# Kernel tuning notes

Hardware: AMD Instinct MI355X
Metric: run time of the kernel (lower is better)

Reference implementation:

```python
import jax, jax.numpy as jnp
import numpy as np

N_NODES = 100000
N_EDGES = 1600000
IN_DIM = 75
H_COMP = 64
H_BOND = 16
DEPTH = 3


def setup_inputs() -> dict:
    key = jax.random.key(0)
    ks = jax.random.split(key, 8)
    x = jax.random.normal(ks[0], (N_NODES, IN_DIM), dtype=jnp.float32)
    edge_index = jax.random.randint(ks[1], (2, N_EDGES), 0, N_NODES, dtype=jnp.int64)
    edge_attr = jax.random.normal(ks[2], (N_EDGES, H_BOND), dtype=jnp.float32)
    proj_w = jax.random.normal(ks[3], (IN_DIM, H_COMP), dtype=jnp.float32) * (1.0 / np.sqrt(IN_DIM))
    proj_b = jnp.zeros((H_COMP,), dtype=jnp.float32)
    u2_w = jax.random.normal(ks[4], (DEPTH, H_COMP + H_BOND, H_COMP), dtype=jnp.float32) * (1.0 / np.sqrt(H_COMP + H_BOND))
    u2_b = jnp.zeros((DEPTH, H_COMP), dtype=jnp.float32)
    u1_w = jax.random.normal(ks[5], (DEPTH, 2 * H_COMP, H_COMP), dtype=jnp.float32) * (1.0 / np.sqrt(2 * H_COMP))
    u1_b = jnp.zeros((DEPTH, H_COMP), dtype=jnp.float32)
    return {"x": x, "edge_index": edge_index, "edge_attr": edge_attr,
            "proj_w": proj_w, "proj_b": proj_b,
            "u2_w": u2_w, "u2_b": u2_b, "u1_w": u1_w, "u1_b": u1_b}


def reference(x, edge_index, edge_attr, proj_w, proj_b, u2_w, u2_b, u1_w, u1_b):
    # PyG default flow source_to_target: messages gathered from edge_index[0],
    # scatter-added at edge_index[1].
    src, dst = edge_index[0], edge_index[1]
    n = x.shape[0]
    # input projection: [N, in_dim] -> [N, H]
    h = x @ proj_w + proj_b
    for l in range(u2_w.shape[0]):
        # message: concat(x_j, edge_attr) -> Linear -> LeakyReLU(0.1)   [E, H+B] -> [E, H]
        z = jnp.concatenate([h[src], edge_attr], axis=-1)
        m = jax.nn.leaky_relu(z @ u2_w[l] + u2_b[l], negative_slope=0.1)
        # aggregate: scatter-add over destination nodes  [E, H] -> [N, H]
        agg = jax.ops.segment_sum(m, dst, num_segments=n)
        # update: concat(x, agg) -> Linear  [N, 2H] -> [N, H]
        h = jnp.concatenate([h, agg], axis=-1) @ u1_w[l] + u1_b[l]
    return h
```

## Files before the change

### kernel.cpp

```cpp
#include <hip/hip_runtime.h>

typedef __attribute__((ext_vector_type(8))) short frag_ab;
typedef __attribute__((ext_vector_type(4))) float frag_cd;

__device__ __forceinline__ short f2bf(float f) {
  union { float f; unsigned u; } v; v.f = f;
  unsigned r = v.u + 0x7fffu + ((v.u >> 16) & 1u);
  return (short)(r >> 16);
}
__device__ __forceinline__ float bf2f(short s) {
  union { unsigned u; float f; } v; v.u = ((unsigned)(unsigned short)s) << 16;
  return v.f;
}

__device__ __forceinline__ void wconv_body(
    const float* __restrict__ W, short* __restrict__ out,
    int Keff, int S, int nmat, int tid)
{
  int per = S * 4 * 64;
  if (tid >= nmat * per) return;
  int m = tid / per, r = tid % per;
  int s = r / 256, ct = (r >> 6) & 3, ln = r & 63;
  const float* Wm = W + (size_t)m * Keff * 64;
  __align__(16) short tmp[8];
  for (int j = 0; j < 8; ++j) {
    int k = s * 32 + (ln >> 4) * 8 + j;
    int n = ct * 16 + (ln & 15);
    tmp[j] = (k < Keff) ? f2bf(Wm[k * 64 + n]) : (short)0;
  }
  *(uint4*)&out[((size_t)m * per + (size_t)(s * 4 + ct) * 64 + ln) * 8] = *(uint4*)tmp;
}

__global__ void wconv_all(const float* __restrict__ pw,
                          const float* __restrict__ u2w,
                          const float* __restrict__ u1w,
                          short* projt, short* u2t, short* u1t)
{
  int b = blockIdx.x, t = threadIdx.x;
  if (b < 3)        wconv_body(pw,  projt, 75,  3, 1, b * 256 + t);
  else if (b < 12)  wconv_body(u2w, u2t,   80,  3, 3, (b - 3) * 256 + t);
  else              wconv_body(u1w, u1t,   128, 4, 3, (b - 12) * 256 + t);
}

#define AS1 104
__global__ __launch_bounds__(256, 4) void proj_kernel(
    const float* __restrict__ x, const short* __restrict__ wt,
    const float* __restrict__ bias, short* __restrict__ hbf, int N)
{
  __shared__ __align__(16) short A[128 * AS1];
  int t = threadIdx.x;
  int nb = blockIdx.x * 128;
  int ln = t & 63;
  frag_ab bf[12];
  for (int s = 0; s < 3; ++s)
    for (int ct = 0; ct < 4; ++ct)
      bf[s * 4 + ct] = *(const frag_ab*)&wt[((size_t)(s * 4 + ct) * 64 + ln) * 8];
  for (int i = 0; i < 48; ++i) {
    int q = i * 256 + t; int el = q / 96; int c = q - el * 96;
    int rg = nb + el;
    float v = (c < 75 && rg < N) ? x[rg * 75 + c] : 0.f;
    A[el * AS1 + c] = f2bf(v);
  }
  __syncthreads();
  int wv = t >> 6;
  int lrow = ln & 15, lk = ln >> 4;
  frag_cd acc[2][4];
  for (int rt = 0; rt < 2; ++rt) for (int ct = 0; ct < 4; ++ct) {
    frag_cd z = {0.f, 0.f, 0.f, 0.f}; acc[rt][ct] = z;
  }
  for (int s = 0; s < 3; ++s) {
    frag_ab a0 = *(const frag_ab*)&A[(wv*32 + lrow) * AS1 + s*32 + lk*8];
    frag_ab a1 = *(const frag_ab*)&A[(wv*32 + 16 + lrow) * AS1 + s*32 + lk*8];
    for (int ct = 0; ct < 4; ++ct) {
      acc[0][ct] = __builtin_amdgcn_mfma_f32_16x16x32_bf16(a0, bf[s*4+ct], acc[0][ct], 0, 0, 0);
      acc[1][ct] = __builtin_amdgcn_mfma_f32_16x16x32_bf16(a1, bf[s*4+ct], acc[1][ct], 0, 0, 0);
    }
  }
  float bv[4];
  for (int ct = 0; ct < 4; ++ct) bv[ct] = bias[ct*16 + lrow];
  for (int rt = 0; rt < 2; ++rt)
    for (int ct = 0; ct < 4; ++ct)
      for (int r = 0; r < 4; ++r) {
        int row = wv*32 + rt*16 + lk*4 + r;
        int rg = nb + row;
        if (rg < N) hbf[(size_t)rg * 64 + ct*16 + lrow] = f2bf(acc[rt][ct][r] + bv[ct]);
      }
}

__global__ __launch_bounds__(256) void hist_kernel(
    const int* __restrict__ dst, const float* __restrict__ attr,
    int* __restrict__ counts, int* __restrict__ rank,
    uint4* __restrict__ abf, int E)
{
  int i = blockIdx.x * 256 + threadIdx.x;
  if (i < E) {
    rank[i] = atomicAdd(&counts[dst[i]], 1);
    const float4* a4 = (const float4*)(attr + (size_t)i * 16);
    float4 v0 = a4[0], v1 = a4[1], v2 = a4[2], v3 = a4[3];
    __align__(16) short tmp[16];
    tmp[0]=f2bf(v0.x); tmp[1]=f2bf(v0.y); tmp[2]=f2bf(v0.z); tmp[3]=f2bf(v0.w);
    tmp[4]=f2bf(v1.x); tmp[5]=f2bf(v1.y); tmp[6]=f2bf(v1.z); tmp[7]=f2bf(v1.w);
    tmp[8]=f2bf(v2.x); tmp[9]=f2bf(v2.y); tmp[10]=f2bf(v2.z); tmp[11]=f2bf(v2.w);
    tmp[12]=f2bf(v3.x); tmp[13]=f2bf(v3.y); tmp[14]=f2bf(v3.z); tmp[15]=f2bf(v3.w);
    uint4* rp = abf + (size_t)i * 2;
    rp[0] = *(uint4*)&tmp[0];
    rp[1] = *(uint4*)&tmp[8];
  }
}

#define SCAN_TILE 2048
__global__ __launch_bounds__(256) void scan_k1(
    const int* __restrict__ counts, int* __restrict__ offsets,
    int* __restrict__ bsum, int n)
{
  __shared__ int ts[256];
  int t = threadIdx.x;
  int base = blockIdx.x * SCAN_TILE + t * 8;
  int v[8]; int s = 0;
  for (int j = 0; j < 8; ++j) { v[j] = (base + j < n) ? counts[base + j] : 0; s += v[j]; }
  ts[t] = s; __syncthreads();
  for (int off = 1; off < 256; off <<= 1) {
    int x = (t >= off) ? ts[t - off] : 0;
    __syncthreads();
    ts[t] += x;
    __syncthreads();
  }
  if (t == 255) bsum[blockIdx.x] = ts[255];
  int run = (t > 0) ? ts[t - 1] : 0;
  for (int j = 0; j < 8; ++j) { if (base + j < n) offsets[base + j] = run; run += v[j]; }
}

__global__ __launch_bounds__(256) void scan_k3(
    int* __restrict__ offsets, const int* __restrict__ bsum, int n, int nb)
{
  __shared__ int adds;
  int t = threadIdx.x;
  if (t < 64) {
    int v = (t < nb) ? bsum[t] : 0;
    int x = v;
    for (int o = 1; o < 64; o <<= 1) { int y = __shfl_up(x, o); if (t >= o) x += y; }
    int b = blockIdx.x;
    int a = __shfl(x, b - 1);
    if (t == 0) adds = (b == 0) ? 0 : a;
  }
  __syncthreads();
  int add = adds;
  int base = blockIdx.x * SCAN_TILE + t;
  for (int j = 0; j < 8; ++j) { int i = base + j * 256; if (i < n) offsets[i] += add; }
}

__global__ __launch_bounds__(256) void scatter_kernel(
    const int* __restrict__ src, const int* __restrict__ dst,
    const int* __restrict__ offsets, const int* __restrict__ rank,
    int4* __restrict__ rec4, int E)
{
  int e = blockIdx.x * 256 + threadIdx.x;
  if (e < E) {
    int d = dst[e];
    int p = offsets[d] + rank[e];
    rec4[p] = make_int4(src[e], d, e, 0);
  }
}

#define MS 66
__global__ __launch_bounds__(256, 6) void msg_kernel(
    const short* __restrict__ hbf, const int4* __restrict__ rec4,
    const uint4* __restrict__ abf,
    const short* __restrict__ wt, const float* __restrict__ bias,
    float* __restrict__ agg, int E)
{
  __shared__ short M2[128 * MS];
  int t = threadIdx.x;
  int eb = blockIdx.x * 128;
  int ln = t & 63;
  int wv = t >> 6;
  int lrow = ln & 15, lk = ln >> 4;
  int lo = wv * 32;

  int g0 = eb + lo + lrow;
  int g1 = g0 + 16;
  int p0 = g0 > E - 1 ? E - 1 : g0;
  int p1 = g1 > E - 1 ? E - 1 : g1;
  int4 sd0 = rec4[p0];
  int4 sd1 = rec4[p1];
  int d0 = (g0 < E) ? sd0.y : -1;
  int d1 = (g1 < E) ? sd1.y : -1;

  frag_ab a[3][2];
  a[0][0] = *(const frag_ab*)&hbf[(size_t)sd0.x * 64 + lk*8];
  a[0][1] = *(const frag_ab*)&hbf[(size_t)sd1.x * 64 + lk*8];
  a[1][0] = *(const frag_ab*)&hbf[(size_t)sd0.x * 64 + 32 + lk*8];
  a[1][1] = *(const frag_ab*)&hbf[(size_t)sd1.x * 64 + 32 + lk*8];
  frag_ab z8 = {0,0,0,0,0,0,0,0};
  a[2][0] = (lk < 2) ? *(const frag_ab*)((const short*)abf + (size_t)sd0.z * 16 + lk*8) : z8;
  a[2][1] = (lk < 2) ? *(const frag_ab*)((const short*)abf + (size_t)sd1.z * 16 + lk*8) : z8;

  frag_cd acc[2][4];
  for (int rt = 0; rt < 2; ++rt) for (int ct = 0; ct < 4; ++ct) {
    frag_cd z = {0.f, 0.f, 0.f, 0.f}; acc[rt][ct] = z;
  }
  for (int s = 0; s < 3; ++s)
    for (int ct = 0; ct < 4; ++ct) {
      frag_ab b = *(const frag_ab*)&wt[((size_t)(s * 4 + ct) * 64 + ln) * 8];
      acc[0][ct] = __builtin_amdgcn_mfma_f32_16x16x32_bf16(a[s][0], b, acc[0][ct], 0, 0, 0);
      acc[1][ct] = __builtin_amdgcn_mfma_f32_16x16x32_bf16(a[s][1], b, acc[1][ct], 0, 0, 0);
    }
  float bv[4];
  for (int ct = 0; ct < 4; ++ct) bv[ct] = bias[ct*16 + lrow];

  for (int rt = 0; rt < 2; ++rt)
    for (int ct = 0; ct < 4; ++ct)
      for (int r = 0; r < 4; ++r) {
        int row = lo + rt*16 + lk*4 + r;
        float m = acc[rt][ct][r] + bv[ct];
        m = m > 0.f ? m : 0.1f * m;
        M2[row * MS + ct*16 + lrow] = f2bf(m);
      }
  __asm__ __volatile__("s_waitcnt lgkmcnt(0)" ::: "memory");

  int dl = (ln < 16) ? d0 : d1;
  int dnext = __shfl_down(dl, 1);
  bool end = (ln < 32) && ((ln == 31) || (dl != dnext));
  unsigned em = (unsigned)__ballot(end);
  unsigned cm = em & ~(em & (0u - em)) & 0x7fffffffu;

  float s = 0.f;
#pragma unroll
  for (int i = 0; i < 32; ++i) {
    s += bf2f(M2[(lo + i) * MS + ln]);
    if ((em >> i) & 1u) {
      int di = (i < 16) ? __shfl(d0, i) : __shfl(d1, i - 16);
      if (di >= 0) {
        float* dest = &agg[(size_t)di * 64 + ln];
        if ((cm >> i) & 1u) *dest = s;
        else unsafeAtomicAdd(dest, s);
      }
      s = 0.f;
    }
  }
}

__global__ __launch_bounds__(256, 4) void upd_kernel(
    const short* __restrict__ hbf, float* __restrict__ agg,
    const short* __restrict__ wt, const float* __restrict__ bias,
    float* __restrict__ hout, short* __restrict__ hbfo, int N, int last)
{
  int t = threadIdx.x;
  int nb = blockIdx.x * 64;
  int ln = t & 63;
  int wv = t >> 6;
  int lrow = ln & 15, lk = ln >> 4;
  int r0 = nb + wv*16 + lrow;

  frag_ab z8 = {0,0,0,0,0,0,0,0};
  frag_ab a[4];
  a[0] = (r0 < N) ? *(const frag_ab*)&hbf[(size_t)r0 * 64 + lk*8]      : z8;
  a[1] = (r0 < N) ? *(const frag_ab*)&hbf[(size_t)r0 * 64 + 32 + lk*8] : z8;
  for (int si = 0; si < 2; ++si) {
    int cb = si * 32 + lk * 8;
    frag_ab af = z8;
    if (r0 < N) {
      float* ap = &agg[(size_t)r0 * 64 + cb];
      float4 v0 = *(const float4*)ap;
      float4 v1 = *(const float4*)(ap + 4);
      af[0]=f2bf(v0.x); af[1]=f2bf(v0.y); af[2]=f2bf(v0.z); af[3]=f2bf(v0.w);
      af[4]=f2bf(v1.x); af[5]=f2bf(v1.y); af[6]=f2bf(v1.z); af[7]=f2bf(v1.w);
      if (!last) {
        float4 z = make_float4(0.f, 0.f, 0.f, 0.f);
        *(float4*)ap = z; *(float4*)(ap + 4) = z;
      }
    }
    a[2 + si] = af;
  }

  frag_cd acc[4];
  for (int ct = 0; ct < 4; ++ct) {
    frag_cd z = {0.f, 0.f, 0.f, 0.f}; acc[ct] = z;
  }
  for (int s = 0; s < 4; ++s)
    for (int ct = 0; ct < 4; ++ct) {
      frag_ab b = *(const frag_ab*)&wt[((size_t)(s * 4 + ct) * 64 + ln) * 8];
      acc[ct] = __builtin_amdgcn_mfma_f32_16x16x32_bf16(a[s], b, acc[ct], 0, 0, 0);
    }
  float bv[4];
  for (int ct = 0; ct < 4; ++ct) bv[ct] = bias[ct*16 + lrow];
  for (int ct = 0; ct < 4; ++ct)
    for (int r = 0; r < 4; ++r) {
      int rg = nb + wv*16 + lk*4 + r;
      if (rg < N) {
        float v = acc[ct][r] + bv[ct];
        if (last) hout[(size_t)rg * 64 + ct*16 + lrow] = v;
        hbfo[(size_t)rg * 64 + ct*16 + lrow] = f2bf(v);
      }
    }
}

extern "C" void kernel_launch(void* const* d_in, const int* in_sizes, int n_in,
                              void* d_out, int out_size, void* d_ws, size_t ws_size,
                              hipStream_t stream) {
  const float* x    = (const float*)d_in[0];
  const int*   ei   = (const int*)d_in[1];
  const float* attr = (const float*)d_in[2];
  const float* pw   = (const float*)d_in[3];
  const float* pb   = (const float*)d_in[4];
  const float* u2w  = (const float*)d_in[5];
  const float* u2b  = (const float*)d_in[6];
  const float* u1w  = (const float*)d_in[7];
  const float* u1b  = (const float*)d_in[8];

  const int N = in_sizes[0] / 75;
  const int E = in_sizes[1] / 2;
  const int* src = ei;
  const int* dst = ei + E;

  float* hout = (float*)d_out;
  char*  ws   = (char*)d_ws;
  size_t nh   = (size_t)N * 64;
  size_t off  = 0;
  short* hbf   = (short*)(ws + off); off += nh * 2;
  float* agg   = (float*)(ws + off); off += nh * 4;
  int4*  rec4  = (int4*)(ws + off);  off += (size_t)E * 16;
  uint4* abf   = (uint4*)(ws + off); off += (size_t)E * 32;
  short* projt = (short*)(ws + off); off += 3 * 4 * 64 * 8 * 2;
  short* u2t   = (short*)(ws + off); off += (size_t)3 * 3 * 4 * 64 * 8 * 2;
  short* u1t   = (short*)(ws + off); off += (size_t)3 * 4 * 4 * 64 * 8 * 2;
  int* counts  = (int*)agg;
  int* offsets = counts + N;
  int* bsum    = offsets + N;
  int* rank    = bsum + 64;

  const int NB = (N + 127) / 128;
  const int NB2 = (N + 63) / 64;
  const int EB = (E + 127) / 128;
  const int GE = (E + 255) / 256;
  const int NS = (N + SCAN_TILE - 1) / SCAN_TILE;

  wconv_all<<<24, 256, 0, stream>>>(pw, u2w, u1w, projt, u2t, u1t);
  proj_kernel<<<NB, 256, 0, stream>>>(x, projt, pb, hbf, N);
  hipMemsetAsync(counts, 0, (size_t)N * 4, stream);
  hist_kernel<<<GE, 256, 0, stream>>>(dst, attr, counts, rank, abf, E);
  scan_k1<<<NS, 256, 0, stream>>>(counts, offsets, bsum, N);
  scan_k3<<<NS, 256, 0, stream>>>(offsets, bsum, N, NS);
  scatter_kernel<<<GE, 256, 0, stream>>>(src, dst, offsets, rank, rec4, E);

  hipMemsetAsync(agg, 0, nh * 4, stream);
  for (int l = 0; l < 3; ++l) {
    msg_kernel<<<EB, 256, 0, stream>>>(hbf, rec4, abf,
                                       u2t + (size_t)l * 6144, u2b + l * 64,
                                       agg, E);
    upd_kernel<<<NB2, 256, 0, stream>>>(hbf, agg,
                                        u1t + (size_t)l * 8192, u1b + l * 64,
                                        hout, hbf, N, l == 2);
  }
}
```

Baseline: 678.5 us.

## Cache dst-sorted edge attributes and remap blocks contiguously per XCD

The first message layer now writes the bf16 edge attributes out in dst-sorted order, so later layers read them contiguously instead of gathering by original edge id. Block indices are remapped so each XCD handles a contiguous range of edges, which improves L2 locality for the gathers and the scatter into agg. The LDS row stride goes from 66 to 68. This costs an extra E*32-byte workspace buffer and an extra write during layer 0.

After: 612.0 us. -9.8%, faster.

```diff
diff --git a/kernel.cpp b/kernel.cpp
--- a/kernel.cpp
+++ b/kernel.cpp
@@ -162,16 +162,21 @@
   }
 }
 
-#define MS 66
+#define MS 68
+template<int SORTSRC>
 __global__ __launch_bounds__(256, 6) void msg_kernel(
     const short* __restrict__ hbf, const int4* __restrict__ rec4,
-    const uint4* __restrict__ abf,
+    const uint4* __restrict__ abf_in, uint4* __restrict__ abf_s,
     const short* __restrict__ wt, const float* __restrict__ bias,
     float* __restrict__ agg, int E)
 {
   __shared__ short M2[128 * MS];
   int t = threadIdx.x;
-  int eb = blockIdx.x * 128;
+  int nwg = gridDim.x, b0 = blockIdx.x;
+  int q = nwg >> 3, r = nwg & 7;
+  int xcd = b0 & 7, bi = b0 >> 3;
+  int b = (xcd < r ? xcd * (q + 1) : r * (q + 1) + (xcd - r) * q) + bi;
+  int eb = b * 128;
   int ln = t & 63;
   int wv = t >> 6;
   int lrow = ln & 15, lk = ln >> 4;
@@ -192,8 +197,20 @@
   a[1][0] = *(const frag_ab*)&hbf[(size_t)sd0.x * 64 + 32 + lk*8];
   a[1][1] = *(const frag_ab*)&hbf[(size_t)sd1.x * 64 + 32 + lk*8];
   frag_ab z8 = {0,0,0,0,0,0,0,0};
-  a[2][0] = (lk < 2) ? *(const frag_ab*)((const short*)abf + (size_t)sd0.z * 16 + lk*8) : z8;
-  a[2][1] = (lk < 2) ? *(const frag_ab*)((const short*)abf + (size_t)sd1.z * 16 + lk*8) : z8;
+  frag_ab at0 = z8, at1 = z8;
+  if (lk < 2) {
+    if (SORTSRC == 0) {
+      at0 = *(const frag_ab*)((const short*)abf_in + (size_t)sd0.z * 16 + lk*8);
+      at1 = *(const frag_ab*)((const short*)abf_in + (size_t)sd1.z * 16 + lk*8);
+      if (g0 < E) *(frag_ab*)((short*)abf_s + (size_t)g0 * 16 + lk*8) = at0;
+      if (g1 < E) *(frag_ab*)((short*)abf_s + (size_t)g1 * 16 + lk*8) = at1;
+    } else {
+      at0 = *(const frag_ab*)((const short*)abf_s + (size_t)p0 * 16 + lk*8);
+      at1 = *(const frag_ab*)((const short*)abf_s + (size_t)p1 * 16 + lk*8);
+    }
+  }
+  a[2][0] = at0;
+  a[2][1] = at1;
 
   frag_cd acc[2][4];
   for (int rt = 0; rt < 2; ++rt) for (int ct = 0; ct < 4; ++ct) {
@@ -201,9 +218,9 @@
   }
   for (int s = 0; s < 3; ++s)
     for (int ct = 0; ct < 4; ++ct) {
-      frag_ab b = *(const frag_ab*)&wt[((size_t)(s * 4 + ct) * 64 + ln) * 8];
-      acc[0][ct] = __builtin_amdgcn_mfma_f32_16x16x32_bf16(a[s][0], b, acc[0][ct], 0, 0, 0);
-      acc[1][ct] = __builtin_amdgcn_mfma_f32_16x16x32_bf16(a[s][1], b, acc[1][ct], 0, 0, 0);
+      frag_ab bb = *(const frag_ab*)&wt[((size_t)(s * 4 + ct) * 64 + ln) * 8];
+      acc[0][ct] = __builtin_amdgcn_mfma_f32_16x16x32_bf16(a[s][0], bb, acc[0][ct], 0, 0, 0);
+      acc[1][ct] = __builtin_amdgcn_mfma_f32_16x16x32_bf16(a[s][1], bb, acc[1][ct], 0, 0, 0);
     }
   float bv[4];
   for (int ct = 0; ct < 4; ++ct) bv[ct] = bias[ct*16 + lrow];
@@ -320,7 +337,8 @@
   short* hbf   = (short*)(ws + off); off += nh * 2;
   float* agg   = (float*)(ws + off); off += nh * 4;
   int4*  rec4  = (int4*)(ws + off);  off += (size_t)E * 16;
-  uint4* abf   = (uint4*)(ws + off); off += (size_t)E * 32;
+  uint4* abf_e = (uint4*)(ws + off); off += (size_t)E * 32;
+  uint4* abf_s = (uint4*)(ws + off); off += (size_t)E * 32;
   short* projt = (short*)(ws + off); off += 3 * 4 * 64 * 8 * 2;
   short* u2t   = (short*)(ws + off); off += (size_t)3 * 3 * 4 * 64 * 8 * 2;
   short* u1t   = (short*)(ws + off); off += (size_t)3 * 4 * 4 * 64 * 8 * 2;
@@ -338,16 +356,20 @@
   wconv_all<<<24, 256, 0, stream>>>(pw, u2w, u1w, projt, u2t, u1t);
   proj_kernel<<<NB, 256, 0, stream>>>(x, projt, pb, hbf, N);
   hipMemsetAsync(counts, 0, (size_t)N * 4, stream);
-  hist_kernel<<<GE, 256, 0, stream>>>(dst, attr, counts, rank, abf, E);
+  hist_kernel<<<GE, 256, 0, stream>>>(dst, attr, counts, rank, abf_e, E);
   scan_k1<<<NS, 256, 0, stream>>>(counts, offsets, bsum, N);
   scan_k3<<<NS, 256, 0, stream>>>(offsets, bsum, N, NS);
   scatter_kernel<<<GE, 256, 0, stream>>>(src, dst, offsets, rank, rec4, E);
 
   hipMemsetAsync(agg, 0, nh * 4, stream);
   for (int l = 0; l < 3; ++l) {
-    msg_kernel<<<EB, 256, 0, stream>>>(hbf, rec4, abf,
-                                       u2t + (size_t)l * 6144, u2b + l * 64,
-                                       agg, E);
+    if (l == 0)
+      msg_kernel<0><<<EB, 256, 0, stream>>>(hbf, rec4, abf_e, abf_s,
+                                            u2t, u2b, agg, E);
+    else
+      msg_kernel<1><<<EB, 256, 0, stream>>>(hbf, rec4, abf_e, abf_s,
+                                            u2t + (size_t)l * 6144, u2b + l * 64,
+                                            agg, E);
     upd_kernel<<<NB2, 256, 0, stream>>>(hbf, agg,
                                         u1t + (size_t)l * 8192, u1b + l * 64,
                                         hout, hbf, N, l == 2);
```
